# Kernel optimization log

Hardware: AMD Instinct MI355X
Metric: run time of the kernel (lower is better)

Reference implementation:

```python
import jax, jax.numpy as jnp
import numpy as np

N_NODES = 50000
N_EDGES = 1_600_000
F_IN = 128
HIDDEN = 128
N_REL = 8
N_GRAPHS = 64


def setup_inputs() -> dict:
    key = jax.random.key(0)
    ks = jax.random.split(key, 16)
    x = jax.random.normal(ks[0], (N_NODES, F_IN), dtype=jnp.float32)
    edge_index = jax.random.randint(ks[1], (2, N_EDGES), 0, N_NODES, dtype=jnp.int32)
    edge_type = jax.random.randint(ks[2], (N_EDGES,), 0, N_REL, dtype=jnp.int32)
    edge_attr = jax.nn.one_hot(edge_type, N_REL, dtype=jnp.float32)  # one-hot relation encoding
    batch = jnp.sort(jax.random.randint(ks[3], (N_NODES,), 0, N_GRAPHS, dtype=jnp.int32))
    s = 1.0 / np.sqrt(F_IN)
    params = {}
    dims = [(F_IN, HIDDEN), (HIDDEN, HIDDEN), (HIDDEN, HIDDEN)]
    for i, (fi, fo) in enumerate(dims, 1):
        params[f"W{i}"] = jax.random.normal(ks[3 + 3 * i], (N_REL, fi, fo), dtype=jnp.float32) * s
        params[f"root{i}"] = jax.random.normal(ks[4 + 3 * i], (fi, fo), dtype=jnp.float32) * s
        params[f"b{i}"] = jnp.zeros((fo,), dtype=jnp.float32)
    lin_w = jax.random.normal(ks[13], (HIDDEN, HIDDEN), dtype=jnp.float32) * (1.0 / np.sqrt(HIDDEN))
    lin_b = jnp.zeros((HIDDEN,), dtype=jnp.float32)
    return {"x": x, "edge_index": edge_index, "edge_attr": edge_attr, "batch": batch,
            **params, "lin_w": lin_w, "lin_b": lin_b}


def _rgcn_conv(x, src, dst, edge_type, W, root, bias):
    # PyG RGCNConv with aggr='mean': per-relation mean of transformed neighbors + root + bias.
    # Mean is linear, so aggregate raw features per (dst, relation) then apply W_r.
    n = x.shape[0]
    seg = dst * N_REL + edge_type                      # combined segment id [E]
    msg = x[src]                                       # [E, F_in] gather
    agg = jax.ops.segment_sum(msg, seg, num_segments=n * N_REL)
    cnt = jax.ops.segment_sum(jnp.ones((src.shape[0],), x.dtype), seg, num_segments=n * N_REL)
    agg = agg / jnp.maximum(cnt, 1.0)[:, None]
    agg = agg.reshape(n, N_REL, -1)                    # [N, R, F_in]
    return jnp.einsum('nri,rio->no', agg, W) + x @ root + bias


def reference(x, edge_index, edge_attr, batch,
              W1, root1, b1, W2, root2, b2, W3, root3, b3, lin_w, lin_b):
    src, dst = edge_index[0], edge_index[1]
    edge_type = jnp.argmax(edge_attr, axis=1)          # np.where(edge_attr == 1)[1]
    h = jax.nn.relu(_rgcn_conv(x, src, dst, edge_type, W1, root1, b1))
    h = jax.nn.relu(_rgcn_conv(h, src, dst, edge_type, W2, root2, b2))
    h = jax.nn.relu(_rgcn_conv(h, src, dst, edge_type, W3, root3, b3))
    # global_mean_pool over graphs
    sums = jax.ops.segment_sum(h, batch, num_segments=N_GRAPHS)
    cnts = jax.ops.segment_sum(jnp.ones((h.shape[0],), h.dtype), batch, num_segments=N_GRAPHS)
    pooled = sums / jnp.maximum(cnts, 1.0)[:, None]    # [G, hidden]
    return pooled @ lin_w + lin_b
```

## Files before the change

kernel.cpp:

```cpp
#include <hip/hip_runtime.h>
#include <hip/hip_fp16.h>

#define N_NODESC 50000
#define N_EDGESC 1600000
#define FEAT 128
#define NREL 8
#define NSEG (N_NODESC * NREL)
#define NGRAPH 64
#define KTOT 1152
#define NKC 36
#define WPACK_ELEMS (NKC * 4 * 128 * 8)
#define WPACK_BLKS (WPACK_ELEMS / 256)
#define NHALF (N_NODESC * FEAT)
#define CVT_BLKS ((NHALF / 4 + 255) / 256)

typedef float f32x4 __attribute__((ext_vector_type(4)));
typedef _Float16 f16x8 __attribute__((ext_vector_type(8)));
typedef unsigned int u32x2 __attribute__((ext_vector_type(2)));
typedef unsigned int u32x4 __attribute__((ext_vector_type(4)));

static inline size_t align256(size_t x) { return (x + 255) & ~(size_t)255; }

__device__ __forceinline__ float4 h4tof4(u32x2 r) {
  const __half* h = (const __half*)&r;
  return make_float4(__half2float(h[0]), __half2float(h[1]),
                     __half2float(h[2]), __half2float(h[3]));
}

__global__ void k_zero(int* __restrict__ p, int n) {
  int i = blockIdx.x * blockDim.x + threadIdx.x;
  int stride = gridDim.x * blockDim.x;
  for (; i < n; i += stride) p[i] = 0;
}

__global__ void k_edge_hist(const int* __restrict__ ei, const float* __restrict__ eattr,
                            int* __restrict__ seg, int* __restrict__ cnt) {
  int e = blockIdx.x * blockDim.x + threadIdx.x;
  if (e >= N_EDGESC) return;
  int dst = ei[N_EDGESC + e];
  const float4* ap = (const float4*)(eattr + (size_t)e * 8);
  float4 a0 = ap[0], a1 = ap[1];
  int ty = 0;
  if (a0.y > 0.5f) ty = 1;
  if (a0.z > 0.5f) ty = 2;
  if (a0.w > 0.5f) ty = 3;
  if (a1.x > 0.5f) ty = 4;
  if (a1.y > 0.5f) ty = 5;
  if (a1.z > 0.5f) ty = 6;
  if (a1.w > 0.5f) ty = 7;
  int s = dst * NREL + ty;
  seg[e] = s;
  atomicAdd(&cnt[s], 1);
}

__global__ void k_scan1(const int* __restrict__ cnt, int* __restrict__ outIncl,
                        int* __restrict__ bsums, int n) {
  __shared__ int sd[256];
  int t = threadIdx.x;
  int base = blockIdx.x * 4096 + t * 16;
  int v[16];
  int s = 0;
#pragma unroll
  for (int j = 0; j < 16; ++j) {
    int idx = base + j;
    int x = (idx < n) ? cnt[idx] : 0;
    s += x;
    v[j] = s;
  }
  sd[t] = s;
  __syncthreads();
  for (int off = 1; off < 256; off <<= 1) {
    int add = (t >= off) ? sd[t - off] : 0;
    __syncthreads();
    sd[t] += add;
    __syncthreads();
  }
  int prev = (t > 0) ? sd[t - 1] : 0;
#pragma unroll
  for (int j = 0; j < 16; ++j) {
    int idx = base + j;
    if (idx < n) outIncl[idx] = prev + v[j];
  }
  if (t == 255) bsums[blockIdx.x] = sd[255];
}

__global__ void k_scan2(int* __restrict__ bsums, int nb) {
  __shared__ int sd[128];
  int t = threadIdx.x;
  int v = (t < nb) ? bsums[t] : 0;
  sd[t] = v;
  __syncthreads();
  for (int off = 1; off < 128; off <<= 1) {
    int add = (t >= off) ? sd[t - off] : 0;
    __syncthreads();
    sd[t] += add;
    __syncthreads();
  }
  if (t < nb) bsums[t] = sd[t] - v;
}

__global__ void k_scan3(int* __restrict__ offsets, const int* __restrict__ bsums, int n) {
  int i = blockIdx.x * blockDim.x + threadIdx.x;
  if (i == 0) offsets[0] = 0;
  if (i < n) offsets[i + 1] += bsums[i >> 12];
}

__global__ void k_scatter(const int* __restrict__ ei, const int* __restrict__ seg,
                          const int* __restrict__ offsets, int* __restrict__ cursor,
                          int* __restrict__ ssrc) {
  int e = blockIdx.x * blockDim.x + threadIdx.x;
  if (e >= N_EDGESC) return;
  int s = seg[e];
  int p = offsets[s] + atomicAdd(&cursor[s], 1);
  ssrc[p] = ei[e];
}

__global__ void k_prep(const float* __restrict__ W1, const float* __restrict__ r1,
                       const float* __restrict__ W2, const float* __restrict__ r2,
                       const float* __restrict__ W3, const float* __restrict__ r3,
                       const float* __restrict__ x,
                       __half* __restrict__ whi3, __half* __restrict__ wlo3,
                       __half* __restrict__ p0) {
  int b = blockIdx.x;
  if (b < 3 * WPACK_BLKS) {
    int L = b / WPACK_BLKS;
    int idx = (b - L * WPACK_BLKS) * 256 + threadIdx.x;
    const float* W = (L == 0) ? W1 : (L == 1) ? W2 : W3;
    const float* root = (L == 0) ? r1 : (L == 1) ? r2 : r3;
    int j = idx & 7;
    int n = (idx >> 3) & 127;
    int slot = idx >> 10;
    int k = slot * 8 + j;
    float v = (k < 1024) ? W[(size_t)k * 128 + n] : root[(size_t)(k - 1024) * 128 + n];
    __half hi = __float2half(v);
    float lof = v - __half2float(hi);
    whi3[(size_t)L * WPACK_ELEMS + idx] = hi;
    wlo3[(size_t)L * WPACK_ELEMS + idx] = __float2half(lof);
  } else {
    int i = (b - 3 * WPACK_BLKS) * 256 + threadIdx.x;
    if (i * 4 < NHALF) {
      float4 v = *(const float4*)&x[i * 4];
      __half h[4] = {__float2half(v.x), __float2half(v.y),
                     __float2half(v.z), __float2half(v.w)};
      *(uint2*)&p0[(size_t)i * 4] = *(uint2*)h;
    }
  }
}

__global__ __launch_bounds__(256, 8) void k_agg(
    const __half* __restrict__ in, const int* __restrict__ offsets,
    const int* __restrict__ ssrc, __half* __restrict__ agg,
    int nodeBase, int nodeCount) {
  int t = blockIdx.x * blockDim.x + threadIdx.x;
  int un = t >> 5;
  int l = t & 31;
  if (un >= nodeCount) return;
  int node = nodeBase + un;
  for (int r = 0; r < NREL; ++r) {
    int sidx = node * NREL + r;
    int beg = offsets[sidx], end = offsets[sidx + 1];
    float4 s = make_float4(0.f, 0.f, 0.f, 0.f);
    for (int base = beg; base < end; base += 4) {
      int last = end - 1;
      int e1 = base + 1 <= last ? base + 1 : last;
      int e2 = base + 2 <= last ? base + 2 : last;
      int e3 = base + 3 <= last ? base + 3 : last;
      int i0 = ssrc[base], i1 = ssrc[e1], i2 = ssrc[e2], i3 = ssrc[e3];
      u32x2 r0 = *(const u32x2*)&in[(size_t)i0 * FEAT + l * 4];
      u32x2 r1 = *(const u32x2*)&in[(size_t)i1 * FEAT + l * 4];
      u32x2 r2 = *(const u32x2*)&in[(size_t)i2 * FEAT + l * 4];
      u32x2 r3 = *(const u32x2*)&in[(size_t)i3 * FEAT + l * 4];
      float4 v0 = h4tof4(r0), v1 = h4tof4(r1), v2 = h4tof4(r2), v3 = h4tof4(r3);
      s.x += v0.x; s.y += v0.y; s.z += v0.z; s.w += v0.w;
      if (base + 1 < end) { s.x += v1.x; s.y += v1.y; s.z += v1.z; s.w += v1.w; }
      if (base + 2 < end) { s.x += v2.x; s.y += v2.y; s.z += v2.z; s.w += v2.w; }
      if (base + 3 < end) { s.x += v3.x; s.y += v3.y; s.z += v3.z; s.w += v3.w; }
    }
    int c = end - beg;
    if (c > 1) {
      float inv = 1.0f / (float)c;
      s.x *= inv; s.y *= inv; s.z *= inv; s.w *= inv;
    }
    __half hv[4] = {__float2half(s.x), __float2half(s.y), __float2half(s.z), __float2half(s.w)};
    __builtin_nontemporal_store(*(u32x2*)hv,
                                (u32x2*)&agg[((size_t)un * NREL + r) * FEAT + l * 4]);
  }
}

__global__ __launch_bounds__(256, 3) void k_gemm_mfma(
    const __half* __restrict__ aggc,
    const __half* __restrict__ xin,
    const __half* __restrict__ Whi, const __half* __restrict__ Wlo,
    const float* __restrict__ bias, __half* __restrict__ out16,
    int n0g, int rows) {
  __shared__ __half Ah[2][4096] __attribute__((aligned(16)));
  __shared__ __half Bh[2][4096] __attribute__((aligned(16)));
  __shared__ __half Bl[2][4096] __attribute__((aligned(16)));

  const int t = threadIdx.x;
  const int lane = t & 63, wave = t >> 6;
  const int l15 = lane & 15, lg = lane >> 4;
  const int wrow0 = wave * 32;
  const int m0 = blockIdx.x * 128;
  const int srow = t >> 1, half = t & 1;

  int rowc = srow;
  if (m0 + rowc >= rows) rowc = rows - 1 - m0;
  if (rowc < 0) rowc = 0;
  const __half* aggRow = aggc + (size_t)(m0 + rowc) * 1024 + half * 16;
  const __half* xRow = xin + (size_t)(n0g + m0 + rowc) * FEAT + half * 16;

  u32x4 av0, av1, sbh0, sbh1, sbl0, sbl1;

#define LOADC(kc)                                                          \
  {                                                                        \
    if ((kc) < 32) {                                                       \
      const u32x4* asrc = (const u32x4*)(aggRow + (kc) * 32);              \
      av0 = __builtin_nontemporal_load(asrc);           \
      av1 = __builtin_nontemporal_load(asrc + 1);                          \
    } else {                                                               \
      const u32x4* asrc = (const u32x4*)(xRow + ((kc) - 32) * 32);         \
      av0 = asrc[0];                                 \
      av1 = asrc[1];                                                       \
    }                                                                      \
    const u32x4* bhs = (const u32x4*)(Whi + (size_t)(kc) * 4096);          \
    const u32x4* bls = (const u32x4*)(Wlo + (size_t)(kc) * 4096);          \
    sbh0 = bhs[t * 2]; sbh1 = bhs[t * 2 + 1];                              \
    sbl0 = bls[t * 2]; sbl1 = bls[t * 2 + 1];                              \
  }
#define WRITEC(b)                                                          \
  {                                                                        \
    int g0 = half * 2;                                                     \
    *(u32x4*)&Ah[b][(g0 * 128 + srow) * 8] = av0;                          \
    *(u32x4*)&Ah[b][((g0 + 1) * 128 + srow) * 8] = av1;                    \
    ((u32x4*)Bh[b])[t * 2] = sbh0; ((u32x4*)Bh[b])[t * 2 + 1] = sbh1;      \
    ((u32x4*)Bl[b])[t * 2] = sbl0; ((u32x4*)Bl[b])[t * 2 + 1] = sbl1;      \
  }

  f32x4 acc[2][8];
#pragma unroll
  for (int a = 0; a < 2; ++a)
#pragma unroll
    for (int b = 0; b < 8; ++b) acc[a][b] = (f32x4){0.f, 0.f, 0.f, 0.f};

  LOADC(0);
  WRITEC(0);
  LOADC(1);
  __syncthreads();

  for (int kc = 0; kc < NKC; ++kc) {
    const int cur = kc & 1;
    f16x8 af[2];
#pragma unroll
    for (int mf = 0; mf < 2; ++mf) {
      int ar = wrow0 + mf * 16 + l15;
      af[mf] = *(const f16x8*)&Ah[cur][(lg * 128 + ar) * 8];
    }
#pragma unroll
    for (int nf = 0; nf < 8; ++nf) {
      int bn = nf * 16 + l15;
      f16x8 vh = *(const f16x8*)&Bh[cur][(lg * 128 + bn) * 8];
      f16x8 vl = *(const f16x8*)&Bl[cur][(lg * 128 + bn) * 8];
      acc[0][nf] = __builtin_amdgcn_mfma_f32_16x16x32_f16(af[0], vh, acc[0][nf], 0, 0, 0);
      acc[0][nf] = __builtin_amdgcn_mfma_f32_16x16x32_f16(af[0], vl, acc[0][nf], 0, 0, 0);
      acc[1][nf] = __builtin_amdgcn_mfma_f32_16x16x32_f16(af[1], vh, acc[1][nf], 0, 0, 0);
      acc[1][nf] = __builtin_amdgcn_mfma_f32_16x16x32_f16(af[1], vl, acc[1][nf], 0, 0, 0);
    }
    if (kc < NKC - 1) {
      WRITEC(cur ^ 1);
      if (kc < NKC - 2) LOADC(kc + 2);
      __syncthreads();
    }
  }
#undef LOADC
#undef WRITEC

  float bcol[8];
#pragma unroll
  for (int nf = 0; nf < 8; ++nf) bcol[nf] = bias[nf * 16 + l15];
#pragma unroll
  for (int mf = 0; mf < 2; ++mf)
#pragma unroll
    for (int nf = 0; nf < 8; ++nf)
#pragma unroll
      for (int j = 0; j < 4; ++j) {
        int grow = m0 + wrow0 + mf * 16 + lg * 4 + j;
        if (grow < rows) {
          float v = acc[mf][nf][j] + bcol[nf];
          v = v > 0.f ? v : 0.f;
          out16[(size_t)(n0g + grow) * FEAT + nf * 16 + l15] = __float2half(v);
        }
      }
}

__global__ void k_pool(const __half* __restrict__ h, const int* __restrict__ batch,
                       const float* __restrict__ lw, const float* __restrict__ lb,
                       float* __restrict__ out) {
  __shared__ float sums[8][128];
  __shared__ float prow[128];
  int gidx = blockIdx.x, t = threadIdx.x;
  int f = t & 127, grp = t >> 7;
  int lo = 0, hi = N_NODESC;
  while (lo < hi) {
    int mid = (lo + hi) >> 1;
    if (batch[mid] < gidx) lo = mid + 1; else hi = mid;
  }
  int start = lo;
  hi = N_NODESC;
  while (lo < hi) {
    int mid = (lo + hi) >> 1;
    if (batch[mid] < gidx + 1) lo = mid + 1; else hi = mid;
  }
  int end = lo;
  float s = 0.f;
  for (int n = start + grp; n < end; n += 8) s += __half2float(h[(size_t)n * FEAT + f]);
  sums[grp][f] = s;
  __syncthreads();
  if (grp == 0) {
    float tot = 0.f;
#pragma unroll
    for (int gg = 0; gg < 8; ++gg) tot += sums[gg][f];
    int c = end - start;
    prow[f] = (c > 0) ? tot / (float)c : 0.f;
  }
  __syncthreads();
  float a = 0.f;
  for (int k = grp * 16; k < grp * 16 + 16; ++k) a = fmaf(prow[k], lw[(size_t)k * FEAT + f], a);
  __syncthreads();
  sums[grp][f] = a;
  __syncthreads();
  if (grp == 0) {
    float tot = lb[f];
#pragma unroll
    for (int gg = 0; gg < 8; ++gg) tot += sums[gg][f];
    out[(size_t)gidx * FEAT + f] = tot;
  }
}

extern "C" void kernel_launch(void* const* d_in, const int* in_sizes, int n_in,
                              void* d_out, int out_size, void* d_ws, size_t ws_size,
                              hipStream_t stream) {
  const float* x = (const float*)d_in[0];
  const int* ei = (const int*)d_in[1];
  const float* eattr = (const float*)d_in[2];
  const int* batch = (const int*)d_in[3];
  const float* Wl[3] = {(const float*)d_in[4], (const float*)d_in[7], (const float*)d_in[10]};
  const float* rl[3] = {(const float*)d_in[5], (const float*)d_in[8], (const float*)d_in[11]};
  const float* bl[3] = {(const float*)d_in[6], (const float*)d_in[9], (const float*)d_in[12]};
  const float* lw = (const float*)d_in[13];
  const float* lb = (const float*)d_in[14];
  float* out = (float*)d_out;
  (void)n_in; (void)in_sizes; (void)out_size;

  size_t pos = 0;
  char* base = (char*)d_ws;
  auto alloc = [&](size_t bytes) { char* q = base + pos; pos += align256(bytes); return q; };
  int* seg = (int*)alloc(sizeof(int) * (size_t)N_EDGESC);
  int* cntcur = (int*)alloc(sizeof(int) * (size_t)2 * NSEG);
  int* cnt = cntcur;
  int* cursor = cntcur + NSEG;
  int* offsets = (int*)alloc(sizeof(int) * (size_t)(NSEG + 1));
  int* bsums = (int*)alloc(sizeof(int) * 1024);
  int* ssrc = (int*)alloc(sizeof(int) * (size_t)N_EDGESC);
  __half* p0 = (__half*)alloc(sizeof(__half) * (size_t)NHALF);
  __half* p1 = (__half*)alloc(sizeof(__half) * (size_t)NHALF);
  __half* whi3 = (__half*)alloc(sizeof(__half) * (size_t)3 * WPACK_ELEMS);
  __half* wlo3 = (__half*)alloc(sizeof(__half) * (size_t)3 * WPACK_ELEMS);
  size_t remain = (ws_size > pos) ? (ws_size - pos) : 0;
  long long cn = (long long)(remain / (sizeof(__half) * NREL * FEAT));
  int chunkNodes = (cn > N_NODESC) ? N_NODESC : (int)cn;
  chunkNodes &= ~127;
  if (chunkNodes < 128) chunkNodes = 128;
  __half* aggbuf = (__half*)(base + pos);
  int nchunks = (N_NODESC + chunkNodes - 1) / chunkNodes;

  hipLaunchKernelGGL(k_zero, dim3(2048), dim3(256), 0, stream, cntcur, 2 * NSEG);
  hipLaunchKernelGGL(k_edge_hist, dim3((N_EDGESC + 255) / 256), dim3(256), 0, stream,
                     ei, eattr, seg, cnt);
  int nbScan = (NSEG + 4095) / 4096;
  hipLaunchKernelGGL(k_scan1, dim3(nbScan), dim3(256), 0, stream, cnt, offsets + 1, bsums, NSEG);
  hipLaunchKernelGGL(k_scan2, dim3(1), dim3(128), 0, stream, bsums, nbScan);
  hipLaunchKernelGGL(k_scan3, dim3((NSEG + 255) / 256), dim3(256), 0, stream, offsets, bsums, NSEG);
  hipLaunchKernelGGL(k_scatter, dim3((N_EDGESC + 255) / 256), dim3(256), 0, stream,
                     ei, seg, offsets, cursor, ssrc);

  hipLaunchKernelGGL(k_prep, dim3(3 * WPACK_BLKS + CVT_BLKS), dim3(256), 0, stream,
                     Wl[0], rl[0], Wl[1], rl[1], Wl[2], rl[2], x, whi3, wlo3, p0);

  const __half* inPtr = p0;
  __half* outPtr = p1;
  for (int L = 0; L < 3; ++L) {
    const __half* whi = whi3 + (size_t)L * WPACK_ELEMS;
    const __half* wlo = wlo3 + (size_t)L * WPACK_ELEMS;
    for (int c = 0; c < nchunks; ++c) {
      int nodeBase = c * chunkNodes;
      int rowsC = N_NODESC - nodeBase;
      if (rowsC > chunkNodes) rowsC = chunkNodes;
      int aggBlocks = (rowsC * 32 + 255) / 256;
      hipLaunchKernelGGL(k_agg, dim3(aggBlocks), dim3(256), 0, stream,
                         inPtr, offsets, ssrc, aggbuf, nodeBase, rowsC);
      hipLaunchKernelGGL(k_gemm_mfma, dim3((rowsC + 127) / 128), dim3(256), 0, stream,
                         aggbuf, inPtr, whi, wlo, bl[L], outPtr, nodeBase, rowsC);
    }
    const __half* tmp = inPtr;
    inPtr = outPtr;
    outPtr = (__half*)tmp;
  }

  hipLaunchKernelGGL(k_pool, dim3(NGRAPH), dim3(1024), 0, stream, p1, batch, lw, lb, out);
}
```

Measured before the change: 755.7 us.

## Build CSR by destination node and accumulate relations in registers

Edges are now sorted into a per-destination-node CSR instead of a per-(node, relation) one, with the relation type packed into the upper bits of the source index. Each aggregation thread walks one node's edge list once and routes every message into one of eight register accumulators. This shrinks the count, scan and offset arrays eightfold and removes the many near-empty segment loops. The zeroing work is folded into the prep kernel, and the nontemporal loads in the GEMM A path are simplified to plain loads. In exchange the aggregation kernel uses more registers (launch bounds lowered to 6), branches on a per-edge switch, and relies on source indices fitting in 16 bits.

```diff
diff --git a/kernel.cpp b/kernel.cpp
--- a/kernel.cpp
+++ b/kernel.cpp
@@ -5,14 +5,13 @@
 #define N_EDGESC 1600000
 #define FEAT 128
 #define NREL 8
-#define NSEG (N_NODESC * NREL)
 #define NGRAPH 64
-#define KTOT 1152
 #define NKC 36
 #define WPACK_ELEMS (NKC * 4 * 128 * 8)
 #define WPACK_BLKS (WPACK_ELEMS / 256)
 #define NHALF (N_NODESC * FEAT)
 #define CVT_BLKS ((NHALF / 4 + 255) / 256)
+#define ZERO_BLKS ((2 * N_NODESC + 1023) / 1024)
 
 typedef float f32x4 __attribute__((ext_vector_type(4)));
 typedef _Float16 f16x8 __attribute__((ext_vector_type(8)));
@@ -27,16 +26,12 @@
                      __half2float(h[2]), __half2float(h[3]));
 }
 
-__global__ void k_zero(int* __restrict__ p, int n) {
-  int i = blockIdx.x * blockDim.x + threadIdx.x;
-  int stride = gridDim.x * blockDim.x;
-  for (; i < n; i += stride) p[i] = 0;
-}
-
 __global__ void k_edge_hist(const int* __restrict__ ei, const float* __restrict__ eattr,
-                            int* __restrict__ seg, int* __restrict__ cnt) {
+                            int* __restrict__ seg, int* __restrict__ pk,
+                            int* __restrict__ cnt) {
   int e = blockIdx.x * blockDim.x + threadIdx.x;
   if (e >= N_EDGESC) return;
+  int src = ei[e];
   int dst = ei[N_EDGESC + e];
   const float4* ap = (const float4*)(eattr + (size_t)e * 8);
   float4 a0 = ap[0], a1 = ap[1];
@@ -48,9 +43,9 @@
   if (a1.y > 0.5f) ty = 5;
   if (a1.z > 0.5f) ty = 6;
   if (a1.w > 0.5f) ty = 7;
-  int s = dst * NREL + ty;
-  seg[e] = s;
-  atomicAdd(&cnt[s], 1);
+  seg[e] = dst;
+  pk[e] = src | (ty << 16);
+  atomicAdd(&cnt[dst], 1);
 }
 
 __global__ void k_scan1(const int* __restrict__ cnt, int* __restrict__ outIncl,
@@ -105,14 +100,14 @@
   if (i < n) offsets[i + 1] += bsums[i >> 12];
 }
 
-__global__ void k_scatter(const int* __restrict__ ei, const int* __restrict__ seg,
+__global__ void k_scatter(const int* __restrict__ seg, const int* __restrict__ pk,
                           const int* __restrict__ offsets, int* __restrict__ cursor,
-                          int* __restrict__ ssrc) {
+                          int* __restrict__ edata) {
   int e = blockIdx.x * blockDim.x + threadIdx.x;
   if (e >= N_EDGESC) return;
   int s = seg[e];
   int p = offsets[s] + atomicAdd(&cursor[s], 1);
-  ssrc[p] = ei[e];
+  edata[p] = pk[e];
 }
 
 __global__ void k_prep(const float* __restrict__ W1, const float* __restrict__ r1,
@@ -120,7 +115,7 @@
                        const float* __restrict__ W3, const float* __restrict__ r3,
                        const float* __restrict__ x,
                        __half* __restrict__ whi3, __half* __restrict__ wlo3,
-                       __half* __restrict__ p0) {
+                       __half* __restrict__ p0, int* __restrict__ cntcur) {
   int b = blockIdx.x;
   if (b < 3 * WPACK_BLKS) {
     int L = b / WPACK_BLKS;
@@ -136,7 +131,7 @@
     float lof = v - __half2float(hi);
     whi3[(size_t)L * WPACK_ELEMS + idx] = hi;
     wlo3[(size_t)L * WPACK_ELEMS + idx] = __float2half(lof);
-  } else {
+  } else if (b < 3 * WPACK_BLKS + CVT_BLKS) {
     int i = (b - 3 * WPACK_BLKS) * 256 + threadIdx.x;
     if (i * 4 < NHALF) {
       float4 v = *(const float4*)&x[i * 4];
@@ -144,47 +139,76 @@
                      __float2half(v.z), __float2half(v.w)};
       *(uint2*)&p0[(size_t)i * 4] = *(uint2*)h;
     }
-  }
-}
-
-__global__ __launch_bounds__(256, 8) void k_agg(
+  } else {
+    int i = (b - 3 * WPACK_BLKS - CVT_BLKS) * 1024 + threadIdx.x;
+#pragma unroll
+    for (int q = 0; q < 4; ++q) {
+      int idx = i + q * 256;
+      if (idx < 2 * N_NODESC) cntcur[idx] = 0;
+    }
+  }
+}
+
+__global__ __launch_bounds__(256, 6) void k_agg(
     const __half* __restrict__ in, const int* __restrict__ offsets,
-    const int* __restrict__ ssrc, __half* __restrict__ agg,
+    const int* __restrict__ edata, __half* __restrict__ agg,
     int nodeBase, int nodeCount) {
   int t = blockIdx.x * blockDim.x + threadIdx.x;
   int un = t >> 5;
   int l = t & 31;
   if (un >= nodeCount) return;
   int node = nodeBase + un;
-  for (int r = 0; r < NREL; ++r) {
-    int sidx = node * NREL + r;
-    int beg = offsets[sidx], end = offsets[sidx + 1];
-    float4 s = make_float4(0.f, 0.f, 0.f, 0.f);
-    for (int base = beg; base < end; base += 4) {
-      int last = end - 1;
-      int e1 = base + 1 <= last ? base + 1 : last;
-      int e2 = base + 2 <= last ? base + 2 : last;
-      int e3 = base + 3 <= last ? base + 3 : last;
-      int i0 = ssrc[base], i1 = ssrc[e1], i2 = ssrc[e2], i3 = ssrc[e3];
-      u32x2 r0 = *(const u32x2*)&in[(size_t)i0 * FEAT + l * 4];
-      u32x2 r1 = *(const u32x2*)&in[(size_t)i1 * FEAT + l * 4];
-      u32x2 r2 = *(const u32x2*)&in[(size_t)i2 * FEAT + l * 4];
-      u32x2 r3 = *(const u32x2*)&in[(size_t)i3 * FEAT + l * 4];
-      float4 v0 = h4tof4(r0), v1 = h4tof4(r1), v2 = h4tof4(r2), v3 = h4tof4(r3);
-      s.x += v0.x; s.y += v0.y; s.z += v0.z; s.w += v0.w;
-      if (base + 1 < end) { s.x += v1.x; s.y += v1.y; s.z += v1.z; s.w += v1.w; }
-      if (base + 2 < end) { s.x += v2.x; s.y += v2.y; s.z += v2.z; s.w += v2.w; }
-      if (base + 3 < end) { s.x += v3.x; s.y += v3.y; s.z += v3.z; s.w += v3.w; }
-    }
-    int c = end - beg;
-    if (c > 1) {
-      float inv = 1.0f / (float)c;
-      s.x *= inv; s.y *= inv; s.z *= inv; s.w *= inv;
-    }
-    __half hv[4] = {__float2half(s.x), __float2half(s.y), __float2half(s.z), __float2half(s.w)};
-    __builtin_nontemporal_store(*(u32x2*)hv,
-                                (u32x2*)&agg[((size_t)un * NREL + r) * FEAT + l * 4]);
-  }
+  int beg = offsets[node], end = offsets[node + 1];
+  float4 a0 = {0, 0, 0, 0}, a1 = a0, a2 = a0, a3 = a0, a4 = a0, a5 = a0, a6 = a0, a7 = a0;
+  int c0 = 0, c1 = 0, c2 = 0, c3 = 0, c4 = 0, c5 = 0, c6 = 0, c7 = 0;
+
+#define ACCSLOT(pv, rv)                                                              \
+  {                                                                                  \
+    float4 v = h4tof4(rv);                                                           \
+    switch ((pv) >> 16) {                                                            \
+      case 0: a0.x += v.x; a0.y += v.y; a0.z += v.z; a0.w += v.w; ++c0; break;       \
+      case 1: a1.x += v.x; a1.y += v.y; a1.z += v.z; a1.w += v.w; ++c1; break;       \
+      case 2: a2.x += v.x; a2.y += v.y; a2.z += v.z; a2.w += v.w; ++c2; break;       \
+      case 3: a3.x += v.x; a3.y += v.y; a3.z += v.z; a3.w += v.w; ++c3; break;       \
+      case 4: a4.x += v.x; a4.y += v.y; a4.z += v.z; a4.w += v.w; ++c4; break;       \
+      case 5: a5.x += v.x; a5.y += v.y; a5.z += v.z; a5.w += v.w; ++c5; break;       \
+      case 6: a6.x += v.x; a6.y += v.y; a6.z += v.z; a6.w += v.w; ++c6; break;       \
+      default: a7.x += v.x; a7.y += v.y; a7.z += v.z; a7.w += v.w; ++c7; break;      \
+    }                                                                                \
+  }
+
+  for (int base = beg; base < end; base += 4) {
+    int last = end - 1;
+    int e1 = base + 1 <= last ? base + 1 : last;
+    int e2 = base + 2 <= last ? base + 2 : last;
+    int e3 = base + 3 <= last ? base + 3 : last;
+    int p0v = edata[base], p1v = edata[e1], p2v = edata[e2], p3v = edata[e3];
+    u32x2 r0 = *(const u32x2*)&in[(size_t)(p0v & 0xFFFF) * FEAT + l * 4];
+    u32x2 r1 = *(const u32x2*)&in[(size_t)(p1v & 0xFFFF) * FEAT + l * 4];
+    u32x2 r2 = *(const u32x2*)&in[(size_t)(p2v & 0xFFFF) * FEAT + l * 4];
+    u32x2 r3 = *(const u32x2*)&in[(size_t)(p3v & 0xFFFF) * FEAT + l * 4];
+    ACCSLOT(p0v, r0);
+    if (base + 1 < end) ACCSLOT(p1v, r1);
+    if (base + 2 < end) ACCSLOT(p2v, r2);
+    if (base + 3 < end) ACCSLOT(p3v, r3);
+  }
+#undef ACCSLOT
+
+  __half* dst = &agg[(size_t)un * (NREL * FEAT) + l * 4];
+#define EMIT(ar, cr, r)                                                              \
+  {                                                                                  \
+    float4 s = ar;                                                                   \
+    if (cr > 1) {                                                                    \
+      float inv = 1.0f / (float)cr;                                                  \
+      s.x *= inv; s.y *= inv; s.z *= inv; s.w *= inv;                                \
+    }                                                                                \
+    __half hv[4] = {__float2half(s.x), __float2half(s.y),                            \
+                    __float2half(s.z), __float2half(s.w)};                           \
+    __builtin_nontemporal_store(*(u32x2*)hv, (u32x2*)(dst + (r) * FEAT));            \
+  }
+  EMIT(a0, c0, 0); EMIT(a1, c1, 1); EMIT(a2, c2, 2); EMIT(a3, c3, 3);
+  EMIT(a4, c4, 4); EMIT(a5, c5, 5); EMIT(a6, c6, 6); EMIT(a7, c7, 7);
+#undef EMIT
 }
 
 __global__ __launch_bounds__(256, 3) void k_gemm_mfma(
@@ -214,15 +238,10 @@
 
 #define LOADC(kc)                                                          \
   {                                                                        \
-    if ((kc) < 32) {                                                       \
-      const u32x4* asrc = (const u32x4*)(aggRow + (kc) * 32);              \
-      av0 = __builtin_nontemporal_load(asrc);           \
-      av1 = __builtin_nontemporal_load(asrc + 1);                          \
-    } else {                                                               \
-      const u32x4* asrc = (const u32x4*)(xRow + ((kc) - 32) * 32);         \
-      av0 = asrc[0];                                 \
-      av1 = asrc[1];                                                       \
-    }                                                                      \
+    const __half* asrc = ((kc) < 32) ? (aggRow + (kc) * 32)                \
+                                     : (xRow + ((kc) - 32) * 32);          \
+    av0 = ((const u32x4*)asrc)[0];                                         \
+    av1 = ((const u32x4*)asrc)[1];                                         \
     const u32x4* bhs = (const u32x4*)(Whi + (size_t)(kc) * 4096);          \
     const u32x4* bls = (const u32x4*)(Wlo + (size_t)(kc) * 4096);          \
     sbh0 = bhs[t * 2]; sbh1 = bhs[t * 2 + 1];                              \
@@ -356,12 +375,13 @@
   char* base = (char*)d_ws;
   auto alloc = [&](size_t bytes) { char* q = base + pos; pos += align256(bytes); return q; };
   int* seg = (int*)alloc(sizeof(int) * (size_t)N_EDGESC);
-  int* cntcur = (int*)alloc(sizeof(int) * (size_t)2 * NSEG);
+  int* pk = (int*)alloc(sizeof(int) * (size_t)N_EDGESC);
+  int* cntcur = (int*)alloc(sizeof(int) * (size_t)2 * N_NODESC);
   int* cnt = cntcur;
-  int* cursor = cntcur + NSEG;
-  int* offsets = (int*)alloc(sizeof(int) * (size_t)(NSEG + 1));
+  int* cursor = cntcur + N_NODESC;
+  int* offsets = (int*)alloc(sizeof(int) * (size_t)(N_NODESC + 1));
   int* bsums = (int*)alloc(sizeof(int) * 1024);
-  int* ssrc = (int*)alloc(sizeof(int) * (size_t)N_EDGESC);
+  int* edata = (int*)alloc(sizeof(int) * (size_t)N_EDGESC);
   __half* p0 = (__half*)alloc(sizeof(__half) * (size_t)NHALF);
   __half* p1 = (__half*)alloc(sizeof(__half) * (size_t)NHALF);
   __half* whi3 = (__half*)alloc(sizeof(__half) * (size_t)3 * WPACK_ELEMS);
@@ -374,18 +394,18 @@
   __half* aggbuf = (__half*)(base + pos);
   int nchunks = (N_NODESC + chunkNodes - 1) / chunkNodes;
 
-  hipLaunchKernelGGL(k_zero, dim3(2048), dim3(256), 0, stream, cntcur, 2 * NSEG);
+  hipLaunchKernelGGL(k_prep, dim3(3 * WPACK_BLKS + CVT_BLKS + ZERO_BLKS), dim3(256), 0, stream,
+                     Wl[0], rl[0], Wl[1], rl[1], Wl[2], rl[2], x, whi3, wlo3, p0, cntcur);
   hipLaunchKernelGGL(k_edge_hist, dim3((N_EDGESC + 255) / 256), dim3(256), 0, stream,
-                     ei, eattr, seg, cnt);
-  int nbScan = (NSEG + 4095) / 4096;
-  hipLaunchKernelGGL(k_scan1, dim3(nbScan), dim3(256), 0, stream, cnt, offsets + 1, bsums, NSEG);
+                     ei, eattr, seg, pk, cnt);
+  int nbScan = (N_NODESC + 4095) / 4096;
+  hipLaunchKernelGGL(k_scan1, dim3(nbScan), dim3(256), 0, stream, cnt, offsets + 1, bsums,
+                     N_NODESC);
   hipLaunchKernelGGL(k_scan2, dim3(1), dim3(128), 0, stream, bsums, nbScan);
-  hipLaunchKernelGGL(k_scan3, dim3((NSEG + 255) / 256), dim3(256), 0, stream, offsets, bsums, NSEG);
+  hipLaunchKernelGGL(k_scan3, dim3((N_NODESC + 255) / 256), dim3(256), 0, stream,
+                     offsets, bsums, N_NODESC);
   hipLaunchKernelGGL(k_scatter, dim3((N_EDGESC + 255) / 256), dim3(256), 0, stream,
-                     ei, seg, offsets, cursor, ssrc);
-
-  hipLaunchKernelGGL(k_prep, dim3(3 * WPACK_BLKS + CVT_BLKS), dim3(256), 0, stream,
-                     Wl[0], rl[0], Wl[1], rl[1], Wl[2], rl[2], x, whi3, wlo3, p0);
+                     seg, pk, offsets, cursor, edata);
 
   const __half* inPtr = p0;
   __half* outPtr = p1;
@@ -398,7 +418,7 @@
       if (rowsC > chunkNodes) rowsC = chunkNodes;
       int aggBlocks = (rowsC * 32 + 255) / 256;
       hipLaunchKernelGGL(k_agg, dim3(aggBlocks), dim3(256), 0, stream,
-                         inPtr, offsets, ssrc, aggbuf, nodeBase, rowsC);
+                         inPtr, offsets, edata, aggbuf, nodeBase, rowsC);
       hipLaunchKernelGGL(k_gemm_mfma, dim3((rowsC + 127) / 128), dim3(256), 0, stream,
                          aggbuf, inPtr, whi, wlo, bl[L], outPtr, nodeBase, rowsC);
     }
```

Measured after the change: 1.620 ms. 2.14x slower.
